# Optimization experiments

Hardware: AMD Instinct MI355X
Metric: run time of the kernel (lower is better)

Reference implementation:

```python
import jax, jax.numpy as jnp
import numpy as np

N_PTS = 1_000_000
B = 2048          # number of graphs
C_IN = 8
C_OUT = 32        # `channel` trivial irreps -> conv/activation width
WIDTH = 4.0       # kernel radial width
N_RINGS = 2
EPS = 1e-6


def setup_inputs() -> dict:
    key = jax.random.key(0)
    k = jax.random.split(key, 6)
    x = jax.random.normal(k[0], (N_PTS, C_IN), dtype=jnp.float32)
    coords = jax.random.normal(k[1], (N_PTS, 3), dtype=jnp.float32)
    batch = jnp.sort(jax.random.randint(k[2], (N_PTS,), 0, B))
    # steerable kernel weights: [C_out, C_in, n_rings * n_angular(=4: Y0 + Y1)]
    W = jax.random.normal(k[3], (C_OUT, C_IN, N_RINGS * 4), dtype=jnp.float32) * 0.1
    gamma = jnp.ones((C_OUT,), dtype=jnp.float32)
    beta = jnp.zeros((C_OUT,), dtype=jnp.float32)
    act_bias = jax.random.uniform(k[4], (C_OUT,), dtype=jnp.float32)
    return {"x": x, "coords": coords, "batch": batch, "W": W,
            "gamma": gamma, "beta": beta, "act_bias": act_bias}


def reference(x, coords, batch, W, gamma, beta, act_bias):
    n = x.shape[0]
    # --- global_mean_pool of coords per graph -> out_coords [B,3] ---
    cnt = jax.ops.segment_sum(jnp.ones((n,), x.dtype), batch, num_segments=B)
    cnt = jnp.maximum(cnt, 1.0)
    pos = jax.ops.segment_sum(coords, batch, num_segments=B) / cnt[:, None]
    # --- per-edge relative position: edge i = (point i -> center of graph batch[i]) ---
    rel = pos[batch] - coords                    # [N,3] gather (irregular access)
    d = jnp.linalg.norm(rel, axis=-1)            # [N]
    # --- radial Gaussian ring profile ---
    rings = jnp.linspace(0.0, WIDTH, N_RINGS)
    sigma = WIDTH / max(N_RINGS - 1, 1)
    radial = jnp.exp(-0.5 * ((d[:, None] - rings[None, :]) / sigma) ** 2)   # [N,R]
    # --- angular part: real spherical harmonics l=0 (const) and l=1 (direction) ---
    direc = rel / jnp.maximum(d, EPS)[:, None]
    ang = jnp.concatenate([jnp.ones((n, 1), x.dtype), direc], axis=-1)      # [N,4]
    basis = (radial[:, :, None] * ang[:, None, :]).reshape(n, -1)           # [N, R*4]
    # --- continuous-kernel point conv: per-edge kernel eval + message ---
    msg = jnp.einsum('eb,oib,ei->eo', basis, W, x)                          # [N,C_out]
    # --- scatter-add aggregation to graph centers ---
    out = jax.ops.segment_sum(msg, batch, num_segments=B)                   # [B,C_out]
    # --- IID batch norm (per-channel, batch statistics) ---
    mu = out.mean(axis=0)
    var = out.var(axis=0)
    out = (out - mu) / jnp.sqrt(var + 1e-5) * gamma + beta
    # --- NormNonLinearity (trivial fields) followed by NormPool: relu(|x| - b) ---
    y = jax.nn.relu(jnp.abs(out) - act_bias)                                # [B,C_out]
    return y
```

## Files before the change

### kernel.cpp

```cpp
#include <hip/hip_runtime.h>


#define RS8_STAGE(M, HALF)                                  \
  {                                                         \
    const bool hi_ = (lane & (M)) != 0;                     \
    _Pragma("unroll")                                       \
    for (int k = 0; k < (HALF); ++k) {                      \
      float send = hi_ ? acc[k] : acc[(HALF) + k];          \
      float keep = hi_ ? acc[(HALF) + k] : acc[k];          \
      acc[k] = keep + __shfl_xor(send, (M), 64);            \
    }                                                       \
  }

__device__ __forceinline__ int rev3(int s) {
  return ((s & 1) << 2) | (s & 2) | ((s & 4) >> 2);
}

__device__ __forceinline__ void basis8(float rx, float ry, float rz,
                                       float* bas) {
  float d2 = rx * rx + ry * ry + rz * rz;
  float d = sqrtf(d2);
  float r0 = __expf(-0.03125f * d2);
  float tt = (d - 4.0f) * 0.25f;
  float r1 = __expf(-0.5f * tt * tt);
  float idm = 1.0f / fmaxf(d, 1e-6f);
  float ax = rx * idm, ay = ry * idm, az = rz * idm;
  bas[0] = r0; bas[1] = r0 * ax; bas[2] = r0 * ay; bas[3] = r0 * az;
  bas[4] = r1; bas[5] = r1 * ax; bas[6] = r1 * ay; bas[7] = r1 * az;
}

__global__ __launch_bounds__(256) void boundary_kernel(
    const int* __restrict__ batch, int* __restrict__ start,
    float* __restrict__ stats, int n, int B) {
  int i = blockIdx.x * blockDim.x + threadIdx.x;
  if (i < 64) stats[i] = 0.0f;
  if (i == 0) {
    int b0 = batch[0];
    for (int g = 0; g <= b0; ++g) start[g] = 0;
  }
  if (i < n - 1) {
    int a = batch[i], b = batch[i + 1];
    for (int g = a + 1; g <= b; ++g) start[g] = i + 1;
  } else if (i == n - 1) {
    int a = batch[n - 1];
    for (int g = a + 1; g <= B; ++g) start[g] = n;
  }
}

__global__ __launch_bounds__(256) void graph_kernel(
    const float* __restrict__ x, const float* __restrict__ coords,
    const int* __restrict__ start, const float* __restrict__ W,
    float* __restrict__ out_raw, int n) {
  __shared__ __align__(16) float pv[4][64][20];
  __shared__ float sredm[4][3];
  __shared__ float sred[4][64];
  __shared__ float sVg[64];
  __shared__ float pre2[4][32];
  __shared__ float smean[3];

  const int g = blockIdx.x;
  const int lo = start[g], hi = start[g + 1];
  const int cnt = hi - lo;
  const int t = threadIdx.x;
  const int lane = t & 63;
  const int wv = t >> 6;

  float s1 = 0.f, s2 = 0.f, s3 = 0.f;
  for (int i = lo + t; i < hi; i += 256) {
    s1 += coords[(size_t)i * 3 + 0];
    s2 += coords[(size_t)i * 3 + 1];
    s3 += coords[(size_t)i * 3 + 2];
  }
#pragma unroll
  for (int m = 1; m < 64; m <<= 1) {
    s1 += __shfl_xor(s1, m, 64);
    s2 += __shfl_xor(s2, m, 64);
    s3 += __shfl_xor(s3, m, 64);
  }
  if (lane == 0) { sredm[wv][0] = s1; sredm[wv][1] = s2; sredm[wv][2] = s3; }
  __syncthreads();
  if (t < 3) {
    smean[t] = (sredm[0][t] + sredm[1][t] + sredm[2][t] + sredm[3][t]) /
               (float)max(cnt, 1);
  }
  __syncthreads();
  const float mx = smean[0], my = smean[1], mz = smean[2];

  const int i8 = lane >> 3;
  const int sub = lane & 7;
  float acc[8];
#pragma unroll
  for (int b = 0; b < 8; ++b) acc[b] = 0.f;

  const int niter = (cnt + 255) >> 8;
  for (int it = 0; it < niter; ++it) {
    const int ip = lo + it * 256 + wv * 64 + lane;
    const bool vp = ip < hi;
    const int ic = min(ip, n - 1);
    float cx = coords[(size_t)ic * 3 + 0];
    float cy = coords[(size_t)ic * 3 + 1];
    float cz = coords[(size_t)ic * 3 + 2];
    float bas[8];
    basis8(mx - cx, my - cy, mz - cz, bas);
    float4 xa = ((const float4*)x)[2 * (size_t)ic];
    float4 xb = ((const float4*)x)[2 * (size_t)ic + 1];
    if (!vp) {
      xa = make_float4(0.f, 0.f, 0.f, 0.f);
      xb = make_float4(0.f, 0.f, 0.f, 0.f);
    }
    float* dst = &pv[wv][lane][0];
    ((float4*)dst)[0] = xa;
    ((float4*)dst)[1] = xb;
    ((float4*)dst)[2] = make_float4(bas[0], bas[1], bas[2], bas[3]);
    ((float4*)dst)[3] = make_float4(bas[4], bas[5], bas[6], bas[7]);
#pragma unroll
    for (int j = 0; j < 8; ++j) {
      const float* src = &pv[wv][8 * j + sub][0];
      float xvv = src[i8];
      float4 b03 = *(const float4*)(src + 8);
      float4 b47 = *(const float4*)(src + 12);
      acc[0] += xvv * b03.x;
      acc[1] += xvv * b03.y;
      acc[2] += xvv * b03.z;
      acc[3] += xvv * b03.w;
      acc[4] += xvv * b47.x;
      acc[5] += xvv * b47.y;
      acc[6] += xvv * b47.z;
      acc[7] += xvv * b47.w;
    }
  }

  RS8_STAGE(1, 4)
  RS8_STAGE(2, 2)
  RS8_STAGE(4, 1)
  sred[wv][i8 * 8 + rev3(sub)] = acc[0];
  __syncthreads();
  if (t < 64) sVg[t] = sred[0][t] + sred[1][t] + sred[2][t] + sred[3][t];
  __syncthreads();

  const int o = t & 31;
  const int part = t >> 5;
  const float* wrow = W + (size_t)o * 64 + part * 8;
  float4 w0 = *(const float4*)(wrow);
  float4 w1 = *(const float4*)(wrow + 4);
  float4 v0 = *(const float4*)(&sVg[part * 8]);
  float4 v1 = *(const float4*)(&sVg[part * 8 + 4]);
  float r = w0.x * v0.x + w0.y * v0.y + w0.z * v0.z + w0.w * v0.w +
            w1.x * v1.x + w1.y * v1.y + w1.z * v1.z + w1.w * v1.w;
  r += __shfl_xor(r, 32, 64);
  if (lane < 32) pre2[wv][o] = r;
  __syncthreads();
  if (t < 32) {
    out_raw[(size_t)g * 32 + t] =
        pre2[0][t] + pre2[1][t] + pre2[2][t] + pre2[3][t];
  }
}

__global__ __launch_bounds__(256) void stats_kernel(
    const float* __restrict__ out_raw, float* __restrict__ stats, int B) {
  __shared__ float red[4][32], redq[4][32];
  const int t = threadIdx.x;
  const int o = t & 31;
  const int lane = t & 63;
  const int wv = t >> 6;
  const int stride = gridDim.x * 256;
  float s = 0.f, q = 0.f;
  for (int e = blockIdx.x * 256 + t; e < B * 32; e += stride) {
    float val = out_raw[e];
    s += val;
    q += val * val;
  }
  s += __shfl_xor(s, 32, 64);
  q += __shfl_xor(q, 32, 64);
  if (lane < 32) { red[wv][o] = s; redq[wv][o] = q; }
  __syncthreads();
  if (t < 32) {
    atomicAdd(&stats[t],      red[0][t] + red[1][t] + red[2][t] + red[3][t]);
    atomicAdd(&stats[32 + t], redq[0][t] + redq[1][t] + redq[2][t] + redq[3][t]);
  }
}

__global__ __launch_bounds__(256) void final_kernel(
    const float* __restrict__ out_raw, const float* __restrict__ stats,
    const float* __restrict__ gamma, const float* __restrict__ beta,
    const float* __restrict__ act_bias, float* __restrict__ out, int B) {
  int t = blockIdx.x * blockDim.x + threadIdx.x;
  if (t >= B * 32) return;
  int o = t & 31;
  float invB = 1.0f / (float)B;
  float mu = stats[o] * invB;
  float var = stats[32 + o] * invB - mu * mu;
  float xn = (out_raw[t] - mu) * rsqrtf(var + 1e-5f) * gamma[o] + beta[o];
  float y = fabsf(xn) - act_bias[o];
  out[t] = fmaxf(y, 0.0f);
}

extern "C" void kernel_launch(void* const* d_in, const int* in_sizes, int n_in,
                              void* d_out, int out_size, void* d_ws, size_t ws_size,
                              hipStream_t stream) {
  const float* x      = (const float*)d_in[0];
  const float* coords = (const float*)d_in[1];
  const int*   batch  = (const int*)d_in[2];
  const float* W      = (const float*)d_in[3];
  const float* gamma  = (const float*)d_in[4];
  const float* beta   = (const float*)d_in[5];
  const float* abias  = (const float*)d_in[6];
  float* out = (float*)d_out;

  int n = in_sizes[2];
  int B = out_size / 32;

  int*   start     = (int*)d_ws;
  int    stats_off = ((B + 1 + 3) / 4) * 4;
  float* stats     = (float*)d_ws + stats_off;
  float* out_raw   = stats + 64;

  boundary_kernel<<<(n + 255) / 256, 256, 0, stream>>>(batch, start, stats, n, B);
  graph_kernel<<<B, 256, 0, stream>>>(x, coords, start, W, out_raw, n);
  stats_kernel<<<64, 256, 0, stream>>>(out_raw, stats, B);
  final_kernel<<<(B * 32 + 255) / 256, 256, 0, stream>>>(out_raw, stats, gamma, beta, abias, out, B);
}
```

Measured before the change: 30.96 us.

## Replace boundary pass with per-block binary search and fuse stats with finalize

Removes the boundary kernel that scanned all of batch. Each graph block now finds its segment bounds with a 64-way ballot-based lower_bound over the sorted batch array. The stats and final kernels are merged: every block redundantly reduces the whole out_raw buffer (2048x32 floats) with float4 loads, then normalizes its own slice. This drops atomics, the stats zeroing and two launches, at the cost of repeated reduction work in each block and a few global reads per search step.

```diff
diff --git a/kernel.cpp b/kernel.cpp
--- a/kernel.cpp
+++ b/kernel.cpp
@@ -29,27 +29,32 @@
   bas[4] = r1; bas[5] = r1 * ax; bas[6] = r1 * ay; bas[7] = r1 * az;
 }
 
-__global__ __launch_bounds__(256) void boundary_kernel(
-    const int* __restrict__ batch, int* __restrict__ start,
-    float* __restrict__ stats, int n, int B) {
-  int i = blockIdx.x * blockDim.x + threadIdx.x;
-  if (i < 64) stats[i] = 0.0f;
-  if (i == 0) {
-    int b0 = batch[0];
-    for (int g = 0; g <= b0; ++g) start[g] = 0;
-  }
-  if (i < n - 1) {
-    int a = batch[i], b = batch[i + 1];
-    for (int g = a + 1; g <= b; ++g) start[g] = i + 1;
-  } else if (i == n - 1) {
-    int a = batch[n - 1];
-    for (int g = a + 1; g <= B; ++g) start[g] = n;
-  }
+__device__ __forceinline__ int lower_bound64(const int* __restrict__ a,
+                                             int n, int key, int lane) {
+  int lo = 0, len = n;
+  while (len > 64) {
+    int chunk = (len + 63) >> 6;
+    int p = lo + lane * chunk;
+    bool c = (p < lo + len) && (a[p] < key);
+    unsigned long long mask = __ballot(c);
+    int m = __popcll(mask);
+    if (m == 0) { len = 0; break; }
+    int nlo = lo + (m - 1) * chunk + 1;
+    int nhi = min(lo + m * chunk, lo + len);
+    lo = nlo;
+    len = nhi - nlo;
+  }
+  if (len > 0) {
+    int p = lo + lane;
+    bool c = (lane < len) && (a[p] < key);
+    lo += __popcll(__ballot(c));
+  }
+  return lo;
 }
 
 __global__ __launch_bounds__(256) void graph_kernel(
     const float* __restrict__ x, const float* __restrict__ coords,
-    const int* __restrict__ start, const float* __restrict__ W,
+    const int* __restrict__ batch, const float* __restrict__ W,
     float* __restrict__ out_raw, int n) {
   __shared__ __align__(16) float pv[4][64][20];
   __shared__ float sredm[4][3];
@@ -57,13 +62,20 @@
   __shared__ float sVg[64];
   __shared__ float pre2[4][32];
   __shared__ float smean[3];
+  __shared__ int sbound[2];
 
   const int g = blockIdx.x;
-  const int lo = start[g], hi = start[g + 1];
-  const int cnt = hi - lo;
   const int t = threadIdx.x;
   const int lane = t & 63;
   const int wv = t >> 6;
+
+  if (wv < 2) {
+    int r = lower_bound64(batch, n, g + wv, lane);
+    if (lane == 0) sbound[wv] = r;
+  }
+  __syncthreads();
+  const int lo = sbound[0], hi = sbound[1];
+  const int cnt = hi - lo;
 
   float s1 = 0.f, s2 = 0.f, s3 = 0.f;
   for (int i = lo + t; i < hi; i += 256) {
@@ -156,43 +168,68 @@
   }
 }
 
-__global__ __launch_bounds__(256) void stats_kernel(
-    const float* __restrict__ out_raw, float* __restrict__ stats, int B) {
-  __shared__ float red[4][32], redq[4][32];
+__global__ __launch_bounds__(256) void statsfinal_kernel(
+    const float* __restrict__ out_raw, const float* __restrict__ gamma,
+    const float* __restrict__ beta, const float* __restrict__ act_bias,
+    float* __restrict__ out, int B) {
+  __shared__ float red[4][8][4], redq[4][8][4];
+  __shared__ float sscale[32], sshift[32], sbias[32];
   const int t = threadIdx.x;
-  const int o = t & 31;
   const int lane = t & 63;
   const int wv = t >> 6;
-  const int stride = gridDim.x * 256;
-  float s = 0.f, q = 0.f;
-  for (int e = blockIdx.x * 256 + t; e < B * 32; e += stride) {
-    float val = out_raw[e];
-    s += val;
-    q += val * val;
-  }
-  s += __shfl_xor(s, 32, 64);
-  q += __shfl_xor(q, 32, 64);
-  if (lane < 32) { red[wv][o] = s; redq[wv][o] = q; }
+  const int total = B * 32;
+
+  float s0 = 0.f, s1 = 0.f, s2 = 0.f, s3 = 0.f;
+  float q0 = 0.f, q1 = 0.f, q2 = 0.f, q3 = 0.f;
+  const int n4 = total >> 2;
+  for (int e4 = t; e4 < n4; e4 += 256) {
+    float4 vv = ((const float4*)out_raw)[e4];
+    s0 += vv.x; q0 += vv.x * vv.x;
+    s1 += vv.y; q1 += vv.y * vv.y;
+    s2 += vv.z; q2 += vv.z * vv.z;
+    s3 += vv.w; q3 += vv.w * vv.w;
+  }
+#pragma unroll
+  for (int m = 8; m < 64; m <<= 1) {
+    s0 += __shfl_xor(s0, m, 64); q0 += __shfl_xor(q0, m, 64);
+    s1 += __shfl_xor(s1, m, 64); q1 += __shfl_xor(q1, m, 64);
+    s2 += __shfl_xor(s2, m, 64); q2 += __shfl_xor(q2, m, 64);
+    s3 += __shfl_xor(s3, m, 64); q3 += __shfl_xor(q3, m, 64);
+  }
+  if (lane < 8) {
+    red[wv][lane][0] = s0; redq[wv][lane][0] = q0;
+    red[wv][lane][1] = s1; redq[wv][lane][1] = q1;
+    red[wv][lane][2] = s2; redq[wv][lane][2] = q2;
+    red[wv][lane][3] = s3; redq[wv][lane][3] = q3;
+  }
   __syncthreads();
   if (t < 32) {
-    atomicAdd(&stats[t],      red[0][t] + red[1][t] + red[2][t] + red[3][t]);
-    atomicAdd(&stats[32 + t], redq[0][t] + redq[1][t] + redq[2][t] + redq[3][t]);
-  }
-}
-
-__global__ __launch_bounds__(256) void final_kernel(
-    const float* __restrict__ out_raw, const float* __restrict__ stats,
-    const float* __restrict__ gamma, const float* __restrict__ beta,
-    const float* __restrict__ act_bias, float* __restrict__ out, int B) {
-  int t = blockIdx.x * blockDim.x + threadIdx.x;
-  if (t >= B * 32) return;
-  int o = t & 31;
-  float invB = 1.0f / (float)B;
-  float mu = stats[o] * invB;
-  float var = stats[32 + o] * invB - mu * mu;
-  float xn = (out_raw[t] - mu) * rsqrtf(var + 1e-5f) * gamma[o] + beta[o];
-  float y = fabsf(xn) - act_bias[o];
-  out[t] = fmaxf(y, 0.0f);
+    const int grp = t >> 2, cmp = t & 3;
+    float ssum = red[0][grp][cmp] + red[1][grp][cmp] +
+                 red[2][grp][cmp] + red[3][grp][cmp];
+    float ssq  = redq[0][grp][cmp] + redq[1][grp][cmp] +
+                 redq[2][grp][cmp] + redq[3][grp][cmp];
+    float invB = 1.0f / (float)B;
+    float mu = ssum * invB;
+    float var = ssq * invB - mu * mu;
+    float sc = rsqrtf(var + 1e-5f) * gamma[t];
+    sscale[t] = sc;
+    sshift[t] = beta[t] - mu * sc;
+    sbias[t]  = act_bias[t];
+  }
+  __syncthreads();
+
+  const int base = (blockIdx.x * 256 + t) * 4;
+  if (base < total) {
+    float4 vv = *(const float4*)(out_raw + base);
+    const int o0 = base & 31;
+    float r0 = fabsf(vv.x * sscale[o0 + 0] + sshift[o0 + 0]) - sbias[o0 + 0];
+    float r1 = fabsf(vv.y * sscale[o0 + 1] + sshift[o0 + 1]) - sbias[o0 + 1];
+    float r2 = fabsf(vv.z * sscale[o0 + 2] + sshift[o0 + 2]) - sbias[o0 + 2];
+    float r3 = fabsf(vv.w * sscale[o0 + 3] + sshift[o0 + 3]) - sbias[o0 + 3];
+    *(float4*)(out + base) = make_float4(fmaxf(r0, 0.f), fmaxf(r1, 0.f),
+                                         fmaxf(r2, 0.f), fmaxf(r3, 0.f));
+  }
 }
 
 extern "C" void kernel_launch(void* const* d_in, const int* in_sizes, int n_in,
@@ -210,13 +247,9 @@
   int n = in_sizes[2];
   int B = out_size / 32;
 
-  int*   start     = (int*)d_ws;
-  int    stats_off = ((B + 1 + 3) / 4) * 4;
-  float* stats     = (float*)d_ws + stats_off;
-  float* out_raw   = stats + 64;
-
-  boundary_kernel<<<(n + 255) / 256, 256, 0, stream>>>(batch, start, stats, n, B);
-  graph_kernel<<<B, 256, 0, stream>>>(x, coords, start, W, out_raw, n);
-  stats_kernel<<<64, 256, 0, stream>>>(out_raw, stats, B);
-  final_kernel<<<(B * 32 + 255) / 256, 256, 0, stream>>>(out_raw, stats, gamma, beta, abias, out, B);
-}
+  float* out_raw = (float*)d_ws;
+
+  graph_kernel<<<B, 256, 0, stream>>>(x, coords, batch, W, out_raw, n);
+  int nblk = (B * 32 + 1023) / 1024;
+  statsfinal_kernel<<<nblk, 256, 0, stream>>>(out_raw, gamma, beta, abias, out, B);
+}
```

New measurement: 40.89 us. 32.1% more time.
